# Kernel optimization log

Measured on AMD Instinct MI355X. Metric: run time of the kernel, lower is better.

## Reference

```python
import jax, jax.numpy as jnp
import numpy as np

D_MODEL = 1024
NUM_HEADS = 16
HEAD_DIM = D_MODEL // NUM_HEADS  # 64
MAX_REL = 512
NUM_EMB = 2 * MAX_REL + 1  # 1025
B, L = 2, 2048


def _glorot(key, shape):
    fan_in, fan_out = shape[0], shape[1]
    lim = jnp.sqrt(6.0 / (fan_in + fan_out))
    return jax.random.uniform(key, shape, jnp.float32, -lim, lim)


def setup_inputs() -> dict:
    key = jax.random.key(0)
    ks = jax.random.split(key, 9)
    return {
        "query": jax.random.normal(ks[0], (B, L, D_MODEL), jnp.float32),
        "key": jax.random.normal(ks[1], (B, L, D_MODEL), jnp.float32),
        "value": jax.random.normal(ks[2], (B, L, D_MODEL), jnp.float32),
        "wq": _glorot(ks[3], (D_MODEL, D_MODEL)), "bq": jnp.zeros((D_MODEL,), jnp.float32),
        "wk": _glorot(ks[4], (D_MODEL, D_MODEL)), "bk": jnp.zeros((D_MODEL,), jnp.float32),
        "wv": _glorot(ks[5], (D_MODEL, D_MODEL)), "bv": jnp.zeros((D_MODEL,), jnp.float32),
        "wo": _glorot(ks[6], (D_MODEL, D_MODEL)), "bo": jnp.zeros((D_MODEL,), jnp.float32),
        "rel_emb": _glorot(ks[7], (NUM_EMB, HEAD_DIM)),
    }


def _split_heads(x):
    b, l, _ = x.shape
    return x.reshape(b, l, NUM_HEADS, HEAD_DIM).transpose(0, 2, 1, 3)  # (b,h,l,d)


def reference(query, key, value, wq, bq, wk, bk, wv, bv, wo, bo, rel_emb):
    q = _split_heads(query @ wq + bq)  # (b,h,l,d)
    k = _split_heads(key @ wk + bk)
    v = _split_heads(value @ wv + bv)

    # content scores: (b,h,l,l)
    content = jnp.einsum('bhid,bhjd->bhij', q, k)

    # relative position scores. Original gathers E[clip(j-i)] -> (L,L,d) then
    # einsum('bhid,ijd->bhij'). Equivalent & cheaper: project q onto all
    # relative embeddings once, then gather along the relative-index axis.
    idx = jnp.arange(q.shape[2])
    final_mat = jnp.clip(idx[None, :] - idx[:, None], -MAX_REL, MAX_REL) + MAX_REL  # (L,L)
    q_rel = jnp.einsum('bhid,rd->bhir', q, rel_emb)  # (b,h,l,num_emb)
    position = jnp.take_along_axis(q_rel, final_mat[None, None, :, :], axis=-1)  # (b,h,l,l)

    scores = (content + position) / jnp.sqrt(jnp.float32(HEAD_DIM))
    weights = jax.nn.softmax(scores, axis=-1)  # no mask, dropout off (inference)
    out = jnp.einsum('bhij,bhjd->bhid', weights, v)  # (b,h,l,d)

    out = out.transpose(0, 2, 1, 3).reshape(query.shape[0], -1, D_MODEL)
    return out @ wo + bo
```

## Files before the change

### kernel.cpp

```cpp
#include <hip/hip_runtime.h>
#include <hip/hip_bf16.h>


typedef __attribute__((ext_vector_type(8))) short short8;
typedef __attribute__((ext_vector_type(4))) float floatx4;

#define L_SEQ 2048
#define D_MODEL 1024
#define NHEAD 16
#define DH 64
#define BH 32
#define MROWS 4096
#define PPAD 92

__device__ inline float b2f(short s) {
    unsigned int u = ((unsigned int)(unsigned short)s) << 16;
    float f; __builtin_memcpy(&f, &u, 4); return f;
}
__device__ inline short f2b(float f) {
    unsigned int u; __builtin_memcpy(&u, &f, 4);
    u += 0x7fffu + ((u >> 16) & 1u);
    return (short)(u >> 16);
}
__device__ inline unsigned int pack2(float a, float b) {
    __hip_bfloat162 h = __float22bfloat162_rn(make_float2(a, b));
    unsigned int u; __builtin_memcpy(&u, &h, 4); return u;
}
__device__ inline void st2(short* p, unsigned int v) {
    __builtin_memcpy(p, &v, 4);
}
__device__ inline void st4(short* p, unsigned int a, unsigned int b) {
    unsigned int v[2] = {a, b}; __builtin_memcpy(p, v, 8);
}
__device__ inline void stf4(short* p, floatx4 v) {
    __builtin_memcpy(p, &v, 16);
}
__device__ inline float ldf(const short* p) {
    float f; __builtin_memcpy(&f, p, 4); return f;
}
__device__ inline void async_cp16(short* lds, const short* g) {
    __builtin_amdgcn_global_load_lds(
        (const __attribute__((address_space(1))) unsigned int*)g,
        (__attribute__((address_space(3))) unsigned int*)lds, 16, 0, 0);
}

__global__ __launch_bounds__(256) void detect_dtype(
        const unsigned short* __restrict__ q, int* __restrict__ flag) {
    __shared__ int s[256];
    int tid = threadIdx.x, cnt = 0;
    for (int i = tid; i < 65536; i += 256)
        if ((q[i] & 0x7F80u) == 0x7F80u) cnt++;
    s[tid] = cnt; __syncthreads();
    for (int st = 128; st; st >>= 1) {
        if (tid < st) s[tid] += s[tid + st];
        __syncthreads();
    }
    if (tid == 0) *flag = (s[0] > 4) ? 1 : 0;
}

__global__ __launch_bounds__(256) void prep_all(
        const void* __restrict__ w0, const void* __restrict__ w1,
        const void* __restrict__ w2, const void* __restrict__ w3,
        const void* __restrict__ bq, const void* __restrict__ bk,
        const void* __restrict__ bv, const void* __restrict__ bo,
        const void* __restrict__ rel,
        const float* __restrict__ q, const float* __restrict__ k,
        const float* __restrict__ v,
        short* __restrict__ WT, float* __restrict__ bias4,
        short* __restrict__ relb,
        short* __restrict__ Cq, short* __restrict__ Ck, short* __restrict__ Cv,
        const int* __restrict__ flagp) {
    const int f32 = *flagp;
    const int id = blockIdx.x;
    const int tid = threadIdx.x;

    if (id < 4096) {
        __shared__ short tile[32][33];
        const int wz = id >> 10, rem = id & 1023;
        const int bx = rem & 31, by = rem >> 5;
        const int tx = tid & 31, ty = tid >> 5;
        const void* src = (wz == 0) ? w0 : (wz == 1) ? w1 : (wz == 2) ? w2 : w3;
        short* d = WT + (size_t)wz * (D_MODEL * D_MODEL);
        int x = bx * 32 + tx;
        int y0 = by * 32;
        for (int yy = ty; yy < 32; yy += 8) {
            size_t idx = (size_t)(y0 + yy) * D_MODEL + x;
            tile[yy][tx] = f32 ? f2b(((const float*)src)[idx])
                               : ((const short*)src)[idx];
        }
        __syncthreads();
        int x0 = bx * 32;
        for (int yy = ty; yy < 32; yy += 8)
            d[(size_t)(x0 + yy) * D_MODEL + y0 + tx] = tile[tx][yy];
    } else if (id < 10240) {
        if (!f32) return;
        const int cid = id - 4096;
        const int z = cid >> 11;
        const int bx = cid & 2047;
        const float* src = (z == 0) ? q : (z == 1) ? k : v;
        short* dst = (z == 0) ? Cq : (z == 1) ? Ck : Cv;
        size_t i8 = ((size_t)bx * 256 + tid) * 8;
        float4 f0 = *(const float4*)(&src[i8]);
        float4 f1 = *(const float4*)(&src[i8 + 4]);
        uint4 s;
        s.x = pack2(f0.x, f0.y); s.y = pack2(f0.z, f0.w);
        s.z = pack2(f1.x, f1.y); s.w = pack2(f1.z, f1.w);
        *(uint4*)(&dst[i8]) = s;
    } else {
        int t = (id - 10240) * 256 + tid;
        if (t < 4096) {
            const void* src = (t < 1024) ? bq : (t < 2048) ? bk
                            : (t < 3072) ? bv : bo;
            int i = t & 1023;
            bias4[t] = f32 ? ((const float*)src)[i] : b2f(((const short*)src)[i]);
        } else if (t < 4096 + 65600) {
            int i = t - 4096;
            relb[i] = f32 ? f2b(((const float*)rel)[i]) : ((const short*)rel)[i];
        }
    }
}

__global__ __launch_bounds__(256) void proj_gemm(
        const void* __restrict__ Aq, const void* __restrict__ Ak,
        const void* __restrict__ Av, const short* __restrict__ Cq,
        const short* __restrict__ Ck, const short* __restrict__ Cv,
        const short* __restrict__ WT, const float* __restrict__ bias4,
        short* __restrict__ Qout, const int* __restrict__ flagp) {
    const int f32 = *flagp;
    const int z = blockIdx.z;
    const short* A_ = f32 ? ((z == 0) ? Cq : (z == 1) ? Ck : Cv)
                          : (const short*)((z == 0) ? Aq : (z == 1) ? Ak : Av);
    const short* BT = WT + (size_t)z * (D_MODEL * D_MODEL);
    const float* bias = bias4 + z * 1024;
    short* C = Qout + (size_t)z * ((size_t)MROWS * D_MODEL);
    const int K = D_MODEL;

    __shared__ short Alds[128 * 64];
    __shared__ short Blds[128 * 64];
    const int tid = threadIdx.x;
    const int w = tid >> 6, lane = tid & 63, cl = lane & 15, quad = lane >> 4;
    const int wr = w >> 1, wc = w & 1;
    int wg = blockIdx.x + 8 * blockIdx.y;
    wg = (wg & 7) * 32 + (wg >> 3);
    const int m0 = (wg >> 3) * 128, n0 = (wg & 7) * 128;
    const int lr = lane >> 3;
    const int lc8 = ((lane & 7) ^ lr) * 8;

    floatx4 acc[4][4];
    for (int i = 0; i < 4; i++)
        for (int j = 0; j < 4; j++)
            acc[i][j] = {0.f, 0.f, 0.f, 0.f};

    for (int k0 = 0; k0 < K; k0 += 64) {
        for (int s = 0; s < 4; s++) {
            int rbase = w * 32 + s * 8;
            async_cp16(&Blds[rbase * 64],
                       &BT[(size_t)(n0 + rbase + lr) * K + k0 + lc8]);
            async_cp16(&Alds[rbase * 64],
                       &A_[(size_t)(m0 + rbase + lr) * K + k0 + lc8]);
        }
        __syncthreads();

        for (int ks = 0; ks < 2; ks++) {
            short8 af[4], bfr[4];
            for (int mt = 0; mt < 4; mt++) {
                int row = wr * 64 + mt * 16 + cl;
                int slot = ((ks * 4 + quad) ^ (row & 7)) * 8;
                af[mt] = *(const short8*)(&Alds[row * 64 + slot]);
            }
            for (int nt = 0; nt < 4; nt++) {
                int row = wc * 64 + nt * 16 + cl;
                int slot = ((ks * 4 + quad) ^ (row & 7)) * 8;
                bfr[nt] = *(const short8*)(&Blds[row * 64 + slot]);
            }
            for (int mt = 0; mt < 4; mt++)
                for (int nt = 0; nt < 4; nt++)
                    acc[mt][nt] = __builtin_amdgcn_mfma_f32_16x16x32_bf16(
                        af[mt], bfr[nt], acc[mt][nt], 0, 0, 0);
        }
        __syncthreads();
    }

    for (int nt = 0; nt < 4; nt++) {
        int n = n0 + wc * 64 + nt * 16 + cl;
        float bv = bias[n];
        int h = n >> 6, d = n & 63;
        for (int mt = 0; mt < 4; mt++) {
            for (int r = 0; r < 4; r++) {
                int m = m0 + wr * 64 + mt * 16 + quad * 4 + r;
                float v = acc[mt][nt][r] + bv;
                int b = m >> 11, i = m & 2047;
                if (z < 2)
                    C[(((size_t)(b * NHEAD + h)) * L_SEQ + i) * DH + d] = f2b(v);
                else
                    C[(((size_t)(b * NHEAD + h)) * DH + d) * L_SEQ + i] = f2b(v);
            }
        }
    }
}

__global__ __launch_bounds__(256) void out_gemm(
        const short* __restrict__ A, const short* __restrict__ BT,
        const float* __restrict__ bias, void* __restrict__ C_,
        const int* __restrict__ flagp) {
    const int f32 = *flagp;
    const int K = D_MODEL, N = D_MODEL;
    __shared__ short Alds[128 * 32];
    __shared__ short Blds[64 * 32];
    const int tid = threadIdx.x;
    const int w = tid >> 6, lane = tid & 63, cl = lane & 15, quad = lane >> 4;
    const int wr = w >> 1, wc = w & 1;
    int wg = blockIdx.x + 16 * blockIdx.y;
    wg = (wg & 7) * 64 + (wg >> 3);
    const int m0 = (wg >> 4) * 128, n0 = (wg & 15) * 64;
    const int grow = lane >> 2, gcol = (lane & 3) * 8;

    floatx4 acc[4][2];
    for (int i = 0; i < 4; i++)
        for (int j = 0; j < 2; j++)
            acc[i][j] = {0.f, 0.f, 0.f, 0.f};

    for (int k0 = 0; k0 < K; k0 += 32) {
        for (int s = 0; s < 2; s++) {
            int r = w * 32 + s * 16;
            async_cp16(&Alds[r * 32], &A[(size_t)(m0 + r + grow) * K + k0 + gcol]);
        }
        {
            int r = w * 16;
            async_cp16(&Blds[r * 32], &BT[(size_t)(n0 + r + grow) * K + k0 + gcol]);
        }
        __syncthreads();

        short8 af[4], bfr[2];
        for (int mt = 0; mt < 4; mt++)
            af[mt] = *(const short8*)(&Alds[(wr * 64 + mt * 16 + cl) * 32 + quad * 8]);
        for (int nt = 0; nt < 2; nt++)
            bfr[nt] = *(const short8*)(&Blds[(wc * 32 + nt * 16 + cl) * 32 + quad * 8]);
        for (int mt = 0; mt < 4; mt++)
            for (int nt = 0; nt < 2; nt++)
                acc[mt][nt] = __builtin_amdgcn_mfma_f32_16x16x32_bf16(
                    af[mt], bfr[nt], acc[mt][nt], 0, 0, 0);
        __syncthreads();
    }

    for (int nt = 0; nt < 2; nt++) {
        int n = n0 + wc * 32 + nt * 16 + cl;
        float bv = bias[n];
        for (int mt = 0; mt < 4; mt++) {
            for (int r = 0; r < 4; r++) {
                int m = m0 + wr * 64 + mt * 16 + quad * 4 + r;
                float v = acc[mt][nt][r] + bv;
                if (f32) ((float*)C_)[(size_t)m * N + n] = v;
                else     ((short*)C_)[(size_t)m * N + n] = f2b(v);
            }
        }
    }
}

__global__ __launch_bounds__(256) void attn_kernel(
        const short* __restrict__ Q, const short* __restrict__ K,
        const short* __restrict__ VT, const short* __restrict__ rel,
        short* __restrict__ out) {
    const int tid = threadIdx.x;
    const int w = tid >> 6, lane = tid & 63, cl = lane & 15, quad = lane >> 4;
    int wg = blockIdx.x + 32 * blockIdx.y;
    wg = (wg & 7) * 128 + (wg >> 3);
    const int bh = wg >> 5, b = bh >> 4, h = bh & 15;
    const int I0 = (wg & 31) * 64;
    const int iw0 = I0 + w * 16;

    const short* Qp = Q + (size_t)bh * L_SEQ * DH;
    const short* Kp = K + (size_t)bh * L_SEQ * DH;
    const short* Vp = VT + (size_t)bh * DH * L_SEQ;

    __shared__ short Klds[64 * 64];
    __shared__ short Vtlds[64 * 64];
    __shared__ short Ulds[4][16 * PPAD * 2];

    short* UW = &Ulds[w][0];

    short8 aq[2];
    for (int c = 0; c < 2; c++)
        aq[c] = *(const short8*)(&Qp[(size_t)(iw0 + cl) * DH + c * 32 + quad * 8]);

    const float SCALE2 = 0.125f * 1.44269504088896340736f;
    const float FMAX = 32.0f;

    float addlo, addhi;
    {
        floatx4 Dc = {0.f, 0.f, 0.f, 0.f};
        int eidx = (cl == 1) ? 1024 : 0;
        for (int c = 0; c < 2; c++) {
            short8 ae = *(const short8*)(&rel[(size_t)eidx * DH + c * 32 + quad * 8]);
            Dc = __builtin_amdgcn_mfma_f32_16x16x32_bf16(ae, aq[c], Dc, 0, 0, 0);
        }
        float pcl = __shfl(Dc[0], cl, 64);
        float pch = __shfl(Dc[1], cl, 64);
        addlo = fmaf(pcl, SCALE2, -FMAX);
        addhi = fmaf(pch, SCALE2, -FMAX);
    }

    floatx4 O[4];
    for (int dt = 0; dt < 4; dt++) O[dt] = {0.f, 0.f, 0.f, 0.f};
    float lsum = 0.f;

    const int srow = tid >> 2;
    const int spair = (tid & 3) * 2;

    for (int j0 = 0; j0 < L_SEQ; j0 += 64) {
        for (int s = 0; s < 2; s++) {
            int chunk = spair + s;
            int pos = chunk ^ (srow & 7);
            *(short8*)(&Klds[srow * 64 + pos * 8]) =
                *(const short8*)(&Kp[(size_t)(j0 + srow) * DH + chunk * 8]);
            *(short8*)(&Vtlds[srow * 64 + pos * 8]) =
                *(const short8*)(&Vp[(size_t)srow * L_SEQ + j0 + chunk * 8]);
        }
        __syncthreads();

        const bool hi_clamp = (j0 - iw0 - 15) >= 512;
        const bool lo_clamp = (j0 + 63 - iw0) <= -512;
        const bool banded = !(hi_clamp || lo_clamp);
        const float addc = hi_clamp ? addhi : addlo;

        floatx4 St[4];
        for (int jt = 0; jt < 4; jt++) {
            St[jt] = {0.f, 0.f, 0.f, 0.f};
            int row = jt * 16 + cl;
            for (int c = 0; c < 2; c++) {
                int pos = ((4 * c + quad) ^ (cl & 7)) * 8;
                short8 bk = *(const short8*)(&Klds[row * 64 + pos]);
                St[jt] = __builtin_amdgcn_mfma_f32_16x16x32_bf16(bk, aq[c], St[jt], 0, 0, 0);
            }
        }

        if (banded) {
            floatx4 Pt[5];
            for (int pt = 0; pt < 5; pt++) Pt[pt] = {0.f, 0.f, 0.f, 0.f};
            const int base = j0 - iw0 - 15;
            for (int pt = 0; pt < 5; pt++) {
                int raw = pt * 16 + cl + base;
                int idx = (raw < -512 ? -512 : (raw > 512 ? 512 : raw)) + 512;
                const short* ep = rel + (size_t)idx * DH;
                for (int c = 0; c < 2; c++) {
                    short8 be = *(const short8*)(&ep[c * 32 + quad * 8]);
                    Pt[pt] = __builtin_amdgcn_mfma_f32_16x16x32_bf16(be, aq[c], Pt[pt], 0, 0, 0);
                }
            }
            for (int pt = 0; pt < 5; pt++) {
                int t = pt * 16 + quad * 4;
                stf4(&UW[(cl * PPAD + t) * 2], Pt[pt]);
            }
            for (int jt = 0; jt < 4; jt++)
                for (int r = 0; r < 4; r++) {
                    int t = jt * 16 + quad * 4 + r - cl + 15;
                    float pos = ldf(&UW[(cl * PPAD + t) * 2]);
                    St[jt][r] = fmaf(St[jt][r], SCALE2, fmaf(pos, SCALE2, -FMAX));
                }
        } else {
            for (int jt = 0; jt < 4; jt++)
                for (int r = 0; r < 4; r++)
                    St[jt][r] = fmaf(St[jt][r], SCALE2, addc);
        }

        for (int jt = 0; jt < 4; jt++)
            for (int r = 0; r < 4; r++) {
                float p = __builtin_amdgcn_exp2f(St[jt][r]);
                St[jt][r] = p;
                lsum += p;
            }

        for (int jt = 0; jt < 4; jt++) {
            int jl = jt * 16 + quad * 4;
            int addr = cl * 64 + ((jl >> 3) ^ (cl & 7)) * 8 + (jl & 7);
            st4(&UW[addr], pack2(St[jt][0], St[jt][1]),
                           pack2(St[jt][2], St[jt][3]));
        }

        for (int c = 0; c < 2; c++) {
            int ppos = ((4 * c + quad) ^ (cl & 7)) * 8;
            short8 bp = *(const short8*)(&UW[cl * 64 + ppos]);
            for (int dt = 0; dt < 4; dt++) {
                int row = dt * 16 + cl;
                int vpos = ((4 * c + quad) ^ (cl & 7)) * 8;
                short8 av = *(const short8*)(&Vtlds[row * 64 + vpos]);
                O[dt] = __builtin_amdgcn_mfma_f32_16x16x32_bf16(av, bp, O[dt], 0, 0, 0);
            }
        }
        __syncthreads();
    }

    lsum += __shfl_xor(lsum, 16, 64);
    lsum += __shfl_xor(lsum, 32, 64);
    float inv = 1.0f / lsum;

    for (int dt = 0; dt < 4; dt++) {
        int jl = dt * 16 + quad * 4;
        int addr = cl * 64 + ((jl >> 3) ^ (cl & 7)) * 8 + (jl & 7);
        st4(&UW[addr], pack2(O[dt][0] * inv, O[dt][1] * inv),
                       pack2(O[dt][2] * inv, O[dt][3] * inv));
    }
    size_t obase = ((size_t)b * L_SEQ + iw0 + cl) * D_MODEL + h * DH;
    for (int s = 0; s < 2; s++) {
        int c2 = quad * 2 + s;
        short8 o = *(const short8*)(&UW[cl * 64 + (c2 ^ (cl & 7)) * 8]);
        *(short8*)(&out[obase + c2 * 8]) = o;
    }
}

extern "C" void kernel_launch(void* const* d_in, const int* in_sizes, int n_in,
                              void* d_out, int out_size, void* d_ws, size_t ws_size,
                              hipStream_t stream) {
    const void* query = d_in[0];
    const void* key   = d_in[1];
    const void* value = d_in[2];
    const void* wq = d_in[3];  const void* bq = d_in[4];
    const void* wk = d_in[5];  const void* bk = d_in[6];
    const void* wv = d_in[7];  const void* bv = d_in[8];
    const void* wo = d_in[9];  const void* bo = d_in[10];
    const void* rel = d_in[11];

    int* flag = (int*)d_ws;
    short* ws = (short*)d_ws + 16;
    const size_t WSZ = (size_t)D_MODEL * D_MODEL;
    const size_t TSZ = (size_t)MROWS * D_MODEL;
    short* WT   = ws;
    short* Qw   = ws + 4 * WSZ;
    short* Kw   = Qw + TSZ;
    short* Vtw  = Kw + TSZ;
    short* Attw = Vtw + TSZ;
    float* bias4 = (float*)(Attw + TSZ);
    short* relb  = (short*)(bias4 + 4096);

    short* Cq = (short*)d_out;
    short* Ck = (short*)d_out + TSZ;
    short* Cv = Attw;

    {
        long qb = (long)in_sizes[0];
        const long FP32B = (long)MROWS * D_MODEL * 4;
        const long BF16B = (long)MROWS * D_MODEL * 2;
        int fhost = (qb == FP32B) ? 1 : (qb == BF16B) ? 0 : -1;
        if (fhost >= 0)
            hipMemsetAsync(flag, fhost, 4, stream);
        else
            detect_dtype<<<1, 256, 0, stream>>>((const unsigned short*)query, flag);
    }

    prep_all<<<10513, 256, 0, stream>>>(
        wq, wk, wv, wo, bq, bk, bv, bo, rel,
        (const float*)query, (const float*)key, (const float*)value,
        WT, bias4, relb, Cq, Ck, Cv, flag);

    proj_gemm<<<dim3(8, 32, 3), 256, 0, stream>>>(query, key, value,
                                                  Cq, Ck, Cv, WT, bias4,
                                                  Qw, flag);

    attn_kernel<<<dim3(L_SEQ / 64, BH), 256, 0, stream>>>(Qw, Kw, Vtw, relb, Attw);

    out_gemm<<<dim3(16, 32), 256, 0, stream>>>(Attw, WT + 3 * WSZ, bias4 + 3072,
                                               d_out, flag);
}
```

Measured before the change: 362.1 us.

## Stage transposed V epilogue through LDS and widen out_gemm K-tile with swizzle

The QKV projection epilogue for the V output (stored transposed) now writes each wave's tile into LDS with an XOR swizzle, then emits coalesced 16-byte row stores instead of scattered 2-byte strided writes. The output projection GEMM doubles its K step to 64 and uses a swizzled LDS layout that matches the QKV kernel, which halves the number of barriers. This adds LDS usage and depends on the LDS being free after the main loop's final sync.

```diff
diff --git a/kernel.cpp b/kernel.cpp
--- a/kernel.cpp
+++ b/kernel.cpp
@@ -181,20 +181,40 @@
         __syncthreads();
     }
 
-    for (int nt = 0; nt < 4; nt++) {
-        int n = n0 + wc * 64 + nt * 16 + cl;
-        float bv = bias[n];
-        int h = n >> 6, d = n & 63;
-        for (int mt = 0; mt < 4; mt++) {
-            for (int r = 0; r < 4; r++) {
-                int m = m0 + wr * 64 + mt * 16 + quad * 4 + r;
-                float v = acc[mt][nt][r] + bv;
-                int b = m >> 11, i = m & 2047;
-                if (z < 2)
+    if (z < 2) {
+        for (int nt = 0; nt < 4; nt++) {
+            int n = n0 + wc * 64 + nt * 16 + cl;
+            float bv = bias[n];
+            int h = n >> 6, d = n & 63;
+            for (int mt = 0; mt < 4; mt++) {
+                for (int r = 0; r < 4; r++) {
+                    int m = m0 + wr * 64 + mt * 16 + quad * 4 + r;
+                    float v = acc[mt][nt][r] + bv;
+                    int b = m >> 11, i = m & 2047;
                     C[(((size_t)(b * NHEAD + h)) * L_SEQ + i) * DH + d] = f2b(v);
-                else
-                    C[(((size_t)(b * NHEAD + h)) * DH + d) * L_SEQ + i] = f2b(v);
-            }
+                }
+            }
+        }
+    } else {
+        short* Wt = (w < 2) ? &Alds[w * 4096] : &Blds[(w - 2) * 4096];
+        for (int nt = 0; nt < 4; nt++) {
+            int d = nt * 16 + cl;
+            float bv = bias[n0 + wc * 64 + nt * 16 + cl];
+            for (int mt = 0; mt < 4; mt++) {
+                int ib = mt * 16 + quad * 4;
+                int addr = d * 64 + (((ib >> 3) ^ (d & 7)) << 3) + (ib & 7);
+                st4(&Wt[addr], pack2(acc[mt][nt][0] + bv, acc[mt][nt][1] + bv),
+                               pack2(acc[mt][nt][2] + bv, acc[mt][nt][3] + bv));
+            }
+        }
+        int hh = (n0 + wc * 64) >> 6;
+        int mA = m0 + wr * 64;
+        int bb = mA >> 11, i0 = mA & 2047;
+        size_t cb = (((size_t)(bb * NHEAD + hh)) * DH + lane) * L_SEQ + i0;
+        for (int c = 0; c < 8; c++) {
+            int slot = ((c ^ (lane & 7)) << 3);
+            short8 o; __builtin_memcpy(&o, &Wt[lane * 64 + slot], 16);
+            *(short8*)(&C[cb + c * 8]) = o;
         }
     }
 }
@@ -205,41 +225,52 @@
         const int* __restrict__ flagp) {
     const int f32 = *flagp;
     const int K = D_MODEL, N = D_MODEL;
-    __shared__ short Alds[128 * 32];
-    __shared__ short Blds[64 * 32];
+    __shared__ short Alds[128 * 64];
+    __shared__ short Blds[64 * 64];
     const int tid = threadIdx.x;
     const int w = tid >> 6, lane = tid & 63, cl = lane & 15, quad = lane >> 4;
     const int wr = w >> 1, wc = w & 1;
     int wg = blockIdx.x + 16 * blockIdx.y;
     wg = (wg & 7) * 64 + (wg >> 3);
     const int m0 = (wg >> 4) * 128, n0 = (wg & 15) * 64;
-    const int grow = lane >> 2, gcol = (lane & 3) * 8;
+    const int lr = lane >> 3;
+    const int lc8 = ((lane & 7) ^ lr) * 8;
 
     floatx4 acc[4][2];
     for (int i = 0; i < 4; i++)
         for (int j = 0; j < 2; j++)
             acc[i][j] = {0.f, 0.f, 0.f, 0.f};
 
-    for (int k0 = 0; k0 < K; k0 += 32) {
+    for (int k0 = 0; k0 < K; k0 += 64) {
+        for (int s = 0; s < 4; s++) {
+            int rbase = w * 32 + s * 8;
+            async_cp16(&Alds[rbase * 64],
+                       &A[(size_t)(m0 + rbase + lr) * K + k0 + lc8]);
+        }
         for (int s = 0; s < 2; s++) {
-            int r = w * 32 + s * 16;
-            async_cp16(&Alds[r * 32], &A[(size_t)(m0 + r + grow) * K + k0 + gcol]);
-        }
-        {
-            int r = w * 16;
-            async_cp16(&Blds[r * 32], &BT[(size_t)(n0 + r + grow) * K + k0 + gcol]);
-        }
-        __syncthreads();
-
-        short8 af[4], bfr[2];
-        for (int mt = 0; mt < 4; mt++)
-            af[mt] = *(const short8*)(&Alds[(wr * 64 + mt * 16 + cl) * 32 + quad * 8]);
-        for (int nt = 0; nt < 2; nt++)
-            bfr[nt] = *(const short8*)(&Blds[(wc * 32 + nt * 16 + cl) * 32 + quad * 8]);
-        for (int mt = 0; mt < 4; mt++)
-            for (int nt = 0; nt < 2; nt++)
-                acc[mt][nt] = __builtin_amdgcn_mfma_f32_16x16x32_bf16(
-                    af[mt], bfr[nt], acc[mt][nt], 0, 0, 0);
+            int rbase = w * 16 + s * 8;
+            async_cp16(&Blds[rbase * 64],
+                       &BT[(size_t)(n0 + rbase + lr) * K + k0 + lc8]);
+        }
+        __syncthreads();
+
+        for (int ks = 0; ks < 2; ks++) {
+            short8 af[4], bfr[2];
+            for (int mt = 0; mt < 4; mt++) {
+                int row = wr * 64 + mt * 16 + cl;
+                int slot = ((ks * 4 + quad) ^ (row & 7)) * 8;
+                af[mt] = *(const short8*)(&Alds[row * 64 + slot]);
+            }
+            for (int nt = 0; nt < 2; nt++) {
+                int row = wc * 32 + nt * 16 + cl;
+                int slot = ((ks * 4 + quad) ^ (row & 7)) * 8;
+                bfr[nt] = *(const short8*)(&Blds[row * 64 + slot]);
+            }
+            for (int mt = 0; mt < 4; mt++)
+                for (int nt = 0; nt < 2; nt++)
+                    acc[mt][nt] = __builtin_amdgcn_mfma_f32_16x16x32_bf16(
+                        af[mt], bfr[nt], acc[mt][nt], 0, 0, 0);
+        }
         __syncthreads();
     }
 
```

Result: no change. 355.1 us (-1.9%).
